# Optimization experiments

Hardware: AMD Instinct MI355X
Metric: run time of the kernel (lower is better)

The kernel has to match this reference:

```python
import jax, jax.numpy as jnp
from jax import lax
import numpy as np

EMA_ALPHA = 0.3
LN_EPS = 1e-5
SW = 5  # center_window_size


def _gelu(x):
    return jax.nn.gelu(x, approximate=False)  # torch nn.GELU default = exact erf


def _layernorm(x, g, b):
    mu = x.mean(-1, keepdims=True)
    var = ((x - mu) ** 2).mean(-1, keepdims=True)
    return (x - mu) * lax.rsqrt(var + LN_EPS) * g + b


def _ema_scan(x, alpha):
    # x: [B, T, C]; x_smooth[t] = lerp(x_smooth[t-1], x[t], alpha)
    x0 = x[:, 0]
    def step(prev, xt):
        s = prev + alpha * (xt - prev)
        return s, s
    _, ys = lax.scan(step, x0, jnp.swapaxes(x[:, 1:], 0, 1))  # [T-1, B, C]
    return jnp.concatenate([x0[:, None], jnp.swapaxes(ys, 0, 1)], axis=1)


def _lstm_dir(x, w_ih, w_hh, b):
    # x: [B, T, Cin]; w_ih: [Cin, 4H]; w_hh: [H, 4H]; b: [4H]. torch gate order i,f,g,o
    B = x.shape[0]
    H = w_hh.shape[0]
    pre = jnp.einsum('btc,ch->bth', x, w_ih) + b  # [B, T, 4H]
    def step(carry, p):
        h, c = carry
        gates = p + h @ w_hh
        i, f, g, o = jnp.split(gates, 4, axis=-1)
        c = jax.nn.sigmoid(f) * c + jax.nn.sigmoid(i) * jnp.tanh(g)
        h = jax.nn.sigmoid(o) * jnp.tanh(c)
        return (h, c), h
    init = (jnp.zeros((B, H), x.dtype), jnp.zeros((B, H), x.dtype))
    _, hs = lax.scan(step, init, jnp.swapaxes(pre, 0, 1))  # [T, B, H]
    return jnp.swapaxes(hs, 0, 1)


def _bilstm(x, wih_f, whh_f, b_f, wih_r, whh_r, b_r):
    fwd = _lstm_dir(x, wih_f, whh_f, b_f)
    bwd = jnp.flip(_lstm_dir(jnp.flip(x, axis=1), wih_r, whh_r, b_r), axis=1)
    return jnp.concatenate([fwd, bwd], axis=-1)  # [B, T, 2H]


def setup_inputs() -> dict:
    key = jax.random.key(0)
    ks = jax.random.split(key, 24)
    B, T, C, BD, O, H = 4096, 31, 768, 128, 12, 64
    AUG = 3 * BD  # 384
    def n(k, shape, s):
        return jax.random.normal(k, shape, dtype=jnp.float32) * s
    return {
        'x': n(ks[0], (B, T, C), 1.0),
        'cls_w': n(ks[1], (C, BD), 0.03), 'cls_b': jnp.zeros((BD,), jnp.float32),
        'delta_w': n(ks[2], (C, BD), 0.03), 'delta_b': jnp.zeros((BD,), jnp.float32),
        'acc_w': n(ks[3], (C, BD), 0.03), 'acc_b': jnp.zeros((BD,), jnp.float32),
        'cls_ln_g': jnp.ones((BD,), jnp.float32), 'cls_ln_b': jnp.zeros((BD,), jnp.float32),
        'delta_ln_g': jnp.ones((BD,), jnp.float32), 'delta_ln_b': jnp.zeros((BD,), jnp.float32),
        'acc_ln_g': jnp.ones((BD,), jnp.float32), 'acc_ln_b': jnp.zeros((BD,), jnp.float32),
        'lin0_w': n(ks[4], (AUG, 256), 0.05), 'lin0_b': jnp.zeros((256,), jnp.float32),
        'gate': jnp.float32(0.2),
        'attn_w': n(ks[5], (2 * H, 1), 0.08), 'attn_b': jnp.zeros((1,), jnp.float32),
        'attn_temp': jnp.float32(1.0),
        'lin1_w': n(ks[6], (C, O), 0.03), 'lin1_b': jnp.zeros((O,), jnp.float32),
        'lin2_w': n(ks[7], (2 * H, O), 0.08), 'lin2_b': jnp.zeros((O,), jnp.float32),
        'lstm_wih_f': n(ks[8], (256, 4 * H), 0.06), 'lstm_whh_f': n(ks[9], (H, 4 * H), 0.12),
        'lstm_b_f': jnp.zeros((4 * H,), jnp.float32),
        'lstm_wih_r': n(ks[10], (256, 4 * H), 0.06), 'lstm_whh_r': n(ks[11], (H, 4 * H), 0.12),
        'lstm_b_r': jnp.zeros((4 * H,), jnp.float32),
    }


def reference(x, cls_w, cls_b, delta_w, delta_b, acc_w, acc_b,
              cls_ln_g, cls_ln_b, delta_ln_g, delta_ln_b, acc_ln_g, acc_ln_b,
              lin0_w, lin0_b, gate, attn_w, attn_b, attn_temp,
              lin1_w, lin1_b, lin2_w, lin2_b,
              lstm_wih_f, lstm_whh_f, lstm_b_f, lstm_wih_r, lstm_whh_r, lstm_b_r):
    T = x.shape[1]
    hsl = T // 2
    l, r = max(0, hsl - SW), min(T, hsl + SW + 1)  # center window [10, 21) for T=31

    # --- robust deltas: EMA smoothing + reflect-padded finite differences ---
    x_smooth = _ema_scan(x, EMA_ALPHA)                       # [B, T, C]
    padded = jnp.pad(x_smooth, ((0, 0), (2, 0), (0, 0)), mode='reflect')  # [B, T+2, C]
    dx = padded[:, 1:] - padded[:, :-1]                       # [B, T+1, C]
    ddx = dx[:, 1:] - dx[:, :-1]                              # [B, T, C]
    delta_stream = dx[:, 1:]                                  # [B, T, C]
    acc_stream = ddx                                          # [B, T, C]

    # --- linear branch: mean of lin1 over center window of smoothed stream ---
    linear_logits = (x_smooth[:, l:r] @ lin1_w + lin1_b).mean(axis=1)  # [B, O]

    # --- bottlenecks (eval mode: dropout identity) + LayerNorms ---
    cls_bn = _layernorm(_gelu(x_smooth @ cls_w + cls_b), cls_ln_g, cls_ln_b)
    delta_bn = _layernorm(_gelu(delta_stream @ delta_w + delta_b), delta_ln_g, delta_ln_b)
    acc_bn = _layernorm(_gelu(acc_stream @ acc_w + acc_b), acc_ln_g, acc_ln_b)
    x_aug = jnp.concatenate([cls_bn, delta_bn, acc_bn], axis=-1)  # [B, T, 384]

    x_lstm = _gelu(x_aug @ lin0_w + lin0_b)                   # [B, T, 256]
    x_lstm = x_lstm - x_lstm.mean(axis=1, keepdims=True)      # center over time (fp32)

    # --- BiLSTM + attention pooling over center window ---
    lstm_out = _bilstm(x_lstm, lstm_wih_f, lstm_whh_f, lstm_b_f,
                       lstm_wih_r, lstm_whh_r, lstm_b_r)      # [B, T, 128]
    window = lstm_out[:, l:r]                                 # [B, W, 128]
    temp = jax.nn.softplus(attn_temp) + 0.001
    scores = (window @ attn_w + attn_b)[..., 0] / temp        # [B, W]
    attn = jax.nn.softmax(scores, axis=1)[..., None]          # [B, W, 1]
    attended = (attn * window).sum(axis=1)                    # [B, 128]
    lstm_logits = attended @ lin2_w + lin2_b                  # [B, O]

    g = jax.nn.sigmoid(gate)
    final_logits = linear_logits + g * (lstm_logits - linear_logits)
    return final_logits, attended
```

## Files before the change

kernel.cpp:

```cpp
#include <hip/hip_runtime.h>
#include <cstdint>
#include <cstddef>


typedef short s8v __attribute__((ext_vector_type(8)));
typedef float f4v __attribute__((ext_vector_type(4)));

__device__ __forceinline__ unsigned short f2bf(float f) {
  union { float f; unsigned int u; } v; v.f = f;
  unsigned int u = v.u;
  return (unsigned short)((u + 0x7fffu + ((u >> 16) & 1u)) >> 16);
}
__device__ __forceinline__ float bf2f(unsigned short h) {
  union { unsigned int u; float f; } v; v.u = ((unsigned int)h) << 16;
  return v.f;
}
__device__ __forceinline__ float fsig(float x) {
  return __fdividef(1.f, 1.f + __expf(-x));
}
__device__ __forceinline__ float ftanh(float x) {
  return 1.f - __fdividef(2.f, 1.f + __expf(2.f * x));
}
__device__ __forceinline__ float fgelu(float x) {
  return 0.5f * x * (1.f + erff(x * 0.70710678118654752f));
}

#define OFF_W1T   0u
#define OFF_W2T   589824u
#define OFF_WIHT  786432u
#define OFF_WHHT  1048576u
#define OFF_XS    1114112u
#define OFF_XW    196149248u
#define OFF_LL    208732160u
#define OFF_WIN   208928768u
#define OFF_XAUG  220463104u
#define OFF_XLSTM 317980672u

__global__ __launch_bounds__(256) void k0_prep(
    const float* __restrict__ cls_w, const float* __restrict__ delta_w,
    const float* __restrict__ acc_w, const float* __restrict__ lin0_w,
    const float* __restrict__ wih_f, const float* __restrict__ wih_r,
    const float* __restrict__ whh_f, const float* __restrict__ whh_r,
    unsigned short* __restrict__ ws) {
  int i = blockIdx.x * 256 + threadIdx.x;
  if (i < 294912) {
    int n = i / 768, k = i - n * 768;
    int seg = n >> 7, nn = n & 127;
    const float* w = seg == 0 ? cls_w : (seg == 1 ? delta_w : acc_w);
    ws[i] = f2bf(w[k * 128 + nn]);
  } else if (i < 393216) {
    int j = i - 294912;
    int n = j / 384, k = j - n * 384;
    ws[i] = f2bf(lin0_w[k * 256 + n]);
  } else if (i < 524288) {
    int j = i - 393216;
    int n = j >> 8, k = j & 255;
    ws[i] = f2bf(n < 256 ? wih_f[k * 256 + n] : wih_r[k * 256 + (n - 256)]);
  } else if (i < 557056) {
    int j = i - 524288;
    int d = j >> 14, rem = j & 16383;
    int n = rem >> 6, k = rem & 63;
    const float* w = d ? whh_r : whh_f;
    ws[i] = f2bf(w[k * 256 + n]);
  }
}

__global__ __launch_bounds__(256) void k1_ema(
    const float* __restrict__ x, unsigned short* __restrict__ xs,
    float* __restrict__ xw) {
  int gid = blockIdx.x * 256 + threadIdx.x;
  int b = gid / 768;
  int c = gid - b * 768;
  size_t base = (size_t)b * 31 * 768 + c;
  float s = x[base];
  xs[base] = f2bf(s);
  float wsum = 0.f;
#pragma unroll
  for (int t = 1; t < 31; ++t) {
    float xv = x[base + t * 768];
    s = s + 0.3f * (xv - s);
    xs[base + t * 768] = f2bf(s);
    if (t >= 10 && t <= 20) wsum += s;
  }
  xw[gid] = wsum * (1.f / 11.f);
}

__global__ __launch_bounds__(64) void k1b_linlog(
    const float* __restrict__ xw, const float* __restrict__ lin1_w,
    const float* __restrict__ lin1_b, float* __restrict__ ll) {
  int b = blockIdx.x;
  int lane = threadIdx.x;
  float p[12];
#pragma unroll
  for (int o = 0; o < 12; ++o) p[o] = 0.f;
  for (int k = lane; k < 768; k += 64) {
    float xv = xw[b * 768 + k];
    const float* w = lin1_w + k * 12;
#pragma unroll
    for (int o = 0; o < 12; ++o) p[o] += xv * w[o];
  }
#pragma unroll
  for (int o = 0; o < 12; ++o) {
    float v = p[o];
#pragma unroll
    for (int s = 1; s < 64; s <<= 1) v += __shfl_xor(v, s, 64);
    p[o] = v;
  }
  if (lane == 0) {
#pragma unroll
    for (int o = 0; o < 12; ++o) ll[b * 12 + o] = p[o] + lin1_b[o];
  }
}

template <int KDIM>
__device__ __forceinline__ void gemm64x128(
    const unsigned short* __restrict__ A, int rowClamp,
    const unsigned short* __restrict__ Bt,
    unsigned short* sA, unsigned short* sB, f4v acc[4][2]) {
  const int tid  = threadIdx.x;
  const int lane = tid & 63;
  const int wv   = tid >> 6;
  const int l15  = lane & 15;
  const int quad = lane >> 4;
#pragma unroll
  for (int mt = 0; mt < 4; ++mt)
#pragma unroll
    for (int nt = 0; nt < 2; ++nt)
      acc[mt][nt] = (f4v){0.f, 0.f, 0.f, 0.f};

  for (int kt = 0; kt < KDIM / 64; ++kt) {
#pragma unroll
    for (int c2 = 0; c2 < 2; ++c2) {
      int id = tid + c2 * 256;
      int row = id >> 3, kc = (id & 7) * 8;
      int gr = row < rowClamp ? row : rowClamp;
      uint4 v = *(const uint4*)(A + (size_t)gr * KDIM + kt * 64 + kc);
      *(uint4*)(&sA[row * 72 + kc]) = v;
    }
#pragma unroll
    for (int c2 = 0; c2 < 4; ++c2) {
      int id = tid + c2 * 256;
      int row = id >> 3, kc = (id & 7) * 8;
      uint4 v = *(const uint4*)(Bt + (size_t)row * KDIM + kt * 64 + kc);
      *(uint4*)(&sB[row * 72 + kc]) = v;
    }
    __syncthreads();
#pragma unroll
    for (int ks = 0; ks < 2; ++ks) {
      s8v af[4], bf[2];
#pragma unroll
      for (int mt = 0; mt < 4; ++mt)
        af[mt] = *(const s8v*)(&sA[(mt * 16 + l15) * 72 + ks * 32 + quad * 8]);
#pragma unroll
      for (int nt = 0; nt < 2; ++nt)
        bf[nt] = *(const s8v*)(&sB[(wv * 32 + nt * 16 + l15) * 72 + ks * 32 + quad * 8]);
#pragma unroll
      for (int mt = 0; mt < 4; ++mt)
#pragma unroll
        for (int nt = 0; nt < 2; ++nt)
          acc[mt][nt] = __builtin_amdgcn_mfma_f32_16x16x32_bf16(af[mt], bf[nt], acc[mt][nt], 0, 0, 0);
    }
    __syncthreads();
  }
}

__device__ __forceinline__ void dump_acc(f4v acc[4][2], float* sP) {
  const int tid  = threadIdx.x;
  const int lane = tid & 63;
  const int wv   = tid >> 6;
  const int l15  = lane & 15;
  const int quad = lane >> 4;
#pragma unroll
  for (int mt = 0; mt < 4; ++mt)
#pragma unroll
    for (int nt = 0; nt < 2; ++nt)
#pragma unroll
      for (int r = 0; r < 4; ++r)
        sP[(mt * 16 + quad * 4 + r) * 132 + wv * 32 + nt * 16 + l15] = acc[mt][nt][r];
}

__device__ __forceinline__ float stencil_gelu(const float* sP, int seg, int row, int t,
                                              int col, const float* __restrict__ bias) {
  const float* p = sP + row * 132 + col;
  float v;
  if (seg == 0) {
    v = p[0];
  } else if (seg == 1) {
    v = (t == 0) ? (p[0] - p[132]) : (p[0] - p[-132]);
  } else {
    if (t == 0)      v = p[0] - 2.f * p[132] + p[264];
    else if (t == 1) v = 2.f * (p[0] - p[-132]);
    else             v = p[0] - 2.f * p[-132] + p[-264];
  }
  return fgelu(v + bias[col]);
}

__global__ __launch_bounds__(256) void k2_aug(
    const unsigned short* __restrict__ xs, const unsigned short* __restrict__ W1t,
    const float* __restrict__ cls_b, const float* __restrict__ delta_b,
    const float* __restrict__ acc_b,
    const float* __restrict__ g0, const float* __restrict__ be0,
    const float* __restrict__ g1, const float* __restrict__ be1,
    const float* __restrict__ g2, const float* __restrict__ be2,
    unsigned short* __restrict__ xaug) {
  __shared__ unsigned short sA[64 * 72];
  __shared__ unsigned short sB[128 * 72];
  __shared__ float sP[64 * 132];
  __shared__ float sMu[64], sRs[64];
  int seg = blockIdx.y;
  int rowBase = blockIdx.x * 62;
  f4v acc[4][2];
  gemm64x128<768>(xs + (size_t)rowBase * 768, 61, W1t + (size_t)seg * 128 * 768, sA, sB, acc);
  dump_acc(acc, sP);
  __syncthreads();
  const float* bias = seg == 0 ? cls_b : (seg == 1 ? delta_b : acc_b);
  const float* lng  = seg == 0 ? g0 : (seg == 1 ? g1 : g2);
  const float* lnb  = seg == 0 ? be0 : (seg == 1 ? be1 : be2);
  int tid = threadIdx.x;
  {
    int row = tid >> 2, q = tid & 3;
    if (row < 62) {
      int bb = row >= 31 ? 1 : 0;
      int t  = row - bb * 31;
      float sum = 0.f, ss = 0.f;
      for (int i = 0; i < 32; ++i) {
        float v = stencil_gelu(sP, seg, row, t, q * 32 + i, bias);
        sum += v; ss += v * v;
      }
      sum += __shfl_xor(sum, 1, 64); sum += __shfl_xor(sum, 2, 64);
      ss  += __shfl_xor(ss,  1, 64); ss  += __shfl_xor(ss,  2, 64);
      float mu = sum * (1.f / 128.f);
      if (q == 0) { sMu[row] = mu; sRs[row] = rsqrtf(ss * (1.f / 128.f) - mu * mu + 1e-5f); }
    }
  }
  __syncthreads();
  for (int idx = tid; idx < 62 * 128; idx += 256) {
    int row = idx >> 7, col = idx & 127;
    int bb = row >= 31 ? 1 : 0;
    int t  = row - bb * 31;
    float v = stencil_gelu(sP, seg, row, t, col, bias);
    float o = (v - sMu[row]) * sRs[row] * lng[col] + lnb[col];
    xaug[(size_t)(rowBase + row) * 384 + seg * 128 + col] = f2bf(o);
  }
}

__global__ __launch_bounds__(256) void k3_lstm_in(
    const unsigned short* __restrict__ xaug, const unsigned short* __restrict__ W2t,
    const float* __restrict__ lin0_b, unsigned short* __restrict__ xlstm) {
  __shared__ unsigned short sA[64 * 72];
  __shared__ unsigned short sB[128 * 72];
  __shared__ float sP[64 * 132];
  __shared__ float sCM[256];
  int by = blockIdx.y;
  int rowBase = blockIdx.x * 62;
  f4v acc[4][2];
  gemm64x128<384>(xaug + (size_t)rowBase * 384, 61, W2t + (size_t)by * 128 * 384, sA, sB, acc);
  dump_acc(acc, sP);
  __syncthreads();
  int tid = threadIdx.x;
  for (int idx = tid; idx < 62 * 128; idx += 256) {
    int row = idx >> 7, col = idx & 127;
    sP[row * 132 + col] = fgelu(sP[row * 132 + col] + lin0_b[by * 128 + col]);
  }
  __syncthreads();
  {
    int bb = tid >> 7, col = tid & 127;
    float s = 0.f;
    for (int tr = 0; tr < 31; ++tr) s += sP[(bb * 31 + tr) * 132 + col];
    sCM[tid] = s * (1.f / 31.f);
  }
  __syncthreads();
  for (int idx = tid; idx < 62 * 128; idx += 256) {
    int row = idx >> 7, col = idx & 127;
    int bb = row >= 31 ? 1 : 0;
    float v = sP[row * 132 + col] - sCM[bb * 128 + col];
    xlstm[(size_t)(rowBase + row) * 256 + by * 128 + col] = f2bf(v);
  }
}

__global__ __launch_bounds__(256) void k3b_pre(
    const unsigned short* __restrict__ xlstm, const unsigned short* __restrict__ Wiht,
    const float* __restrict__ b_f, const float* __restrict__ b_r,
    unsigned short* __restrict__ pre) {
  __shared__ unsigned short sA[64 * 72];
  __shared__ unsigned short sB[128 * 72];
  __shared__ float sP[64 * 132];
  int by = blockIdx.y;
  int rowBase = blockIdx.x * 64;
  f4v acc[4][2];
  gemm64x128<256>(xlstm + (size_t)rowBase * 256, 63, Wiht + (size_t)by * 128 * 256, sA, sB, acc);
  dump_acc(acc, sP);
  __syncthreads();
  int tid = threadIdx.x;
  for (int idx = tid; idx < 64 * 128; idx += 256) {
    int row = idx >> 7, col = idx & 127;
    int gcol = by * 128 + col;
    float bias = gcol < 256 ? b_f[gcol] : b_r[gcol - 256];
    pre[(size_t)(rowBase + row) * 512 + gcol] = f2bf(sP[row * 132 + col] + bias);
  }
}

__global__ __launch_bounds__(256) void k4_lstm(
    const unsigned short* __restrict__ pre, const unsigned short* __restrict__ Whht,
    unsigned short* __restrict__ win) {
  __shared__ unsigned short sW[256 * 72];
  __shared__ unsigned short sH[16 * 72];
  __shared__ float sG[16 * 260];
  int tid = threadIdx.x;
  int dir = blockIdx.y;
  int b0  = blockIdx.x * 16;
  {
    const unsigned short* src = Whht + dir * 16384;
#pragma unroll
    for (int c = 0; c < 8; ++c) {
      int id = tid + c * 256;
      int row = id >> 3, kc = (id & 7) * 8;
      uint4 v = *(const uint4*)(src + row * 64 + kc);
      *(uint4*)(&sW[row * 72 + kc]) = v;
    }
  }
  for (int i = tid; i < 16 * 72; i += 256) sH[i] = 0;
  __syncthreads();

  const int lane = tid & 63, wv = tid >> 6, l15 = lane & 15, quad = lane >> 4;
  const int eb = tid >> 4, jb = (tid & 15) * 4;
  float cs[4] = {0.f, 0.f, 0.f, 0.f};

  for (int t = 0; t < 31; ++t) {
    f4v acc[4];
#pragma unroll
    for (int nt = 0; nt < 4; ++nt) acc[nt] = (f4v){0.f, 0.f, 0.f, 0.f};
#pragma unroll
    for (int ks = 0; ks < 2; ++ks) {
      s8v af = *(const s8v*)(&sH[l15 * 72 + ks * 32 + quad * 8]);
#pragma unroll
      for (int nt = 0; nt < 4; ++nt) {
        int n = wv * 64 + nt * 16 + l15;
        s8v bf = *(const s8v*)(&sW[n * 72 + ks * 32 + quad * 8]);
        acc[nt] = __builtin_amdgcn_mfma_f32_16x16x32_bf16(af, bf, acc[nt], 0, 0, 0);
      }
    }
#pragma unroll
    for (int nt = 0; nt < 4; ++nt)
#pragma unroll
      for (int r = 0; r < 4; ++r)
        sG[(quad * 4 + r) * 260 + wv * 64 + nt * 16 + l15] = acc[nt][r];
    __syncthreads();

    int tt = dir ? 30 - t : t;
    const unsigned short* prow = pre + ((size_t)(b0 + eb) * 31 + tt) * 512 + dir * 256;
    ushort4 pi = *(const ushort4*)(prow + jb);
    ushort4 pf = *(const ushort4*)(prow + 64 + jb);
    ushort4 pg = *(const ushort4*)(prow + 128 + jb);
    ushort4 po = *(const ushort4*)(prow + 192 + jb);
    const float* g = &sG[eb * 260];
    float hv[4];
#pragma unroll
    for (int jj = 0; jj < 4; ++jj) {
      int j = jb + jj;
      float vi = g[j]       + bf2f(jj == 0 ? pi.x : jj == 1 ? pi.y : jj == 2 ? pi.z : pi.w);
      float vf = g[64 + j]  + bf2f(jj == 0 ? pf.x : jj == 1 ? pf.y : jj == 2 ? pf.z : pf.w);
      float vg = g[128 + j] + bf2f(jj == 0 ? pg.x : jj == 1 ? pg.y : jj == 2 ? pg.z : pg.w);
      float vo = g[192 + j] + bf2f(jj == 0 ? po.x : jj == 1 ? po.y : jj == 2 ? po.z : po.w);
      float cc = fsig(vf) * cs[jj] + fsig(vi) * ftanh(vg);
      cs[jj] = cc;
      hv[jj] = fsig(vo) * ftanh(cc);
    }
    ushort4 hb;
    hb.x = f2bf(hv[0]); hb.y = f2bf(hv[1]); hb.z = f2bf(hv[2]); hb.w = f2bf(hv[3]);
    *(ushort4*)(&sH[eb * 72 + jb]) = hb;
    if (tt >= 10 && tt <= 20)
      *(ushort4*)(win + ((size_t)(b0 + eb) * 11 + (tt - 10)) * 128 + dir * 64 + jb) = hb;
    __syncthreads();
  }
}

__global__ __launch_bounds__(256) void k5_attn(
    const unsigned short* __restrict__ win, const float* __restrict__ attn_w,
    const float* __restrict__ attn_b, const float* __restrict__ attn_t,
    const float* __restrict__ lin2_w, const float* __restrict__ lin2_b,
    const float* __restrict__ linlog, const float* __restrict__ gate,
    float* __restrict__ out) {
  __shared__ unsigned short sWin[176 * 128];
  __shared__ float sAw[128];
  __shared__ float sSc[176];
  __shared__ float sAtt[16 * 128];
  int tid = threadIdx.x;
  int b0  = blockIdx.x * 16;
#pragma unroll
  for (int c = 0; c < 11; ++c) {
    int id = tid + c * 256;
    int row = id >> 4, kc = (id & 15) * 8;
    uint4 v = *(const uint4*)(win + ((size_t)b0 * 11 + row) * 128 + kc);
    *(uint4*)(&sWin[row * 128 + kc]) = v;
  }
  if (tid < 128) sAw[tid] = attn_w[tid];
  __syncthreads();
  if (tid < 176) {
    int b = tid / 11, wt = tid - b * 11;
    const unsigned short* w = &sWin[(b * 11 + wt) * 128];
    float dot = 0.f;
    for (int ch = 0; ch < 128; ++ch) dot += bf2f(w[ch]) * sAw[ch];
    float temp = logf(1.f + __expf(attn_t[0])) + 0.001f;
    sSc[tid] = (dot + attn_b[0]) / temp;
  }
  __syncthreads();
  if (tid < 16) {
    float m = -1e30f;
    for (int wt = 0; wt < 11; ++wt) m = fmaxf(m, sSc[tid * 11 + wt]);
    float e[11], sum = 0.f;
    for (int wt = 0; wt < 11; ++wt) { e[wt] = __expf(sSc[tid * 11 + wt] - m); sum += e[wt]; }
    float inv = __fdividef(1.f, sum);
    for (int wt = 0; wt < 11; ++wt) sSc[tid * 11 + wt] = e[wt] * inv;
  }
  __syncthreads();
#pragma unroll
  for (int p = 0; p < 8; ++p) {
    int task = tid + p * 256;
    int b = task >> 7, ch = task & 127;
    float a = 0.f;
    for (int wt = 0; wt < 11; ++wt)
      a += sSc[b * 11 + wt] * bf2f(sWin[(b * 11 + wt) * 128 + ch]);
    sAtt[b * 128 + ch] = a;
    out[49152 + (size_t)(b0 + b) * 128 + ch] = a;
  }
  __syncthreads();
  if (tid < 192) {
    int b = tid / 12, o = tid - b * 12;
    float dot = 0.f;
    for (int ch = 0; ch < 128; ++ch) dot += sAtt[b * 128 + ch] * lin2_w[ch * 12 + o];
    dot += lin2_b[o];
    float lin = linlog[(size_t)(b0 + b) * 12 + o];
    float gg = fsig(gate[0]);
    out[(size_t)(b0 + b) * 12 + o] = lin + gg * (dot - lin);
  }
}

extern "C" void kernel_launch(void* const* d_in, const int* in_sizes, int n_in,
                              void* d_out, int out_size, void* d_ws, size_t ws_size,
                              hipStream_t stream) {
  const float* x       = (const float*)d_in[0];
  const float* cls_w   = (const float*)d_in[1];
  const float* cls_b   = (const float*)d_in[2];
  const float* delta_w = (const float*)d_in[3];
  const float* delta_b = (const float*)d_in[4];
  const float* acc_w   = (const float*)d_in[5];
  const float* acc_b   = (const float*)d_in[6];
  const float* cls_g   = (const float*)d_in[7];
  const float* cls_be  = (const float*)d_in[8];
  const float* del_g   = (const float*)d_in[9];
  const float* del_be  = (const float*)d_in[10];
  const float* accg    = (const float*)d_in[11];
  const float* accbe   = (const float*)d_in[12];
  const float* lin0_b  = (const float*)d_in[14];
  const float* gate    = (const float*)d_in[15];
  const float* attn_w  = (const float*)d_in[16];
  const float* attn_b  = (const float*)d_in[17];
  const float* attn_t  = (const float*)d_in[18];
  const float* lin1_w  = (const float*)d_in[19];
  const float* lin1_b  = (const float*)d_in[20];
  const float* lin2_w  = (const float*)d_in[21];
  const float* lin2_b  = (const float*)d_in[22];
  const float* wih_f   = (const float*)d_in[23];
  const float* whh_f   = (const float*)d_in[24];
  const float* b_f     = (const float*)d_in[25];
  const float* wih_r   = (const float*)d_in[26];
  const float* whh_r   = (const float*)d_in[27];
  const float* b_r     = (const float*)d_in[28];
  const float* lin0_w  = (const float*)d_in[13];

  char* ws = (char*)d_ws;
  unsigned short* W1t   = (unsigned short*)(ws + OFF_W1T);
  unsigned short* W2t   = (unsigned short*)(ws + OFF_W2T);
  unsigned short* Wiht  = (unsigned short*)(ws + OFF_WIHT);
  unsigned short* Whht  = (unsigned short*)(ws + OFF_WHHT);
  unsigned short* XS    = (unsigned short*)(ws + OFF_XS);
  unsigned short* PRE   = XS;
  float*          XW    = (float*)(ws + OFF_XW);
  float*          LL    = (float*)(ws + OFF_LL);
  unsigned short* WIN   = (unsigned short*)(ws + OFF_WIN);
  unsigned short* XAUG  = (unsigned short*)(ws + OFF_XAUG);
  unsigned short* XLSTM = (unsigned short*)(ws + OFF_XLSTM);
  float* out = (float*)d_out;

  k0_prep<<<2176, 256, 0, stream>>>(cls_w, delta_w, acc_w, lin0_w, wih_f, wih_r,
                                    whh_f, whh_r, (unsigned short*)ws);
  k1_ema<<<12288, 256, 0, stream>>>(x, XS, XW);
  k1b_linlog<<<4096, 64, 0, stream>>>(XW, lin1_w, lin1_b, LL);
  k2_aug<<<dim3(2048, 3), 256, 0, stream>>>(XS, W1t, cls_b, delta_b, acc_b,
                                            cls_g, cls_be, del_g, del_be, accg, accbe, XAUG);
  k3_lstm_in<<<dim3(2048, 2), 256, 0, stream>>>(XAUG, W2t, lin0_b, XLSTM);
  k3b_pre<<<dim3(1984, 4), 256, 0, stream>>>(XLSTM, Wiht, b_f, b_r, PRE);
  k4_lstm<<<dim3(256, 2), 256, 0, stream>>>(PRE, Whht, WIN);
  k5_attn<<<256, 256, 0, stream>>>(WIN, attn_w, attn_b, attn_t, lin2_w, lin2_b,
                                   LL, gate, out);
}
```

Before: 1.259 ms.

## Enlarge GEMM tiles to 128x128 with register prefetch and prefetch LSTM pre-activations

The shared GEMM helper now computes 128x128 tiles, with each wave owning a 64x64 quadrant. The next K slice is prefetched into registers while MFMAs run on the current one, and the epilogue buffer aliases the A/B staging memory. k2, k3 and k3b now cover twice as many rows per block and process the epilogue in two chunks, with launch bounds asking for two blocks per CU. The LSTM step kernel loads the next timestep's pre-activations before the barrier, to hide global latency on the sequential path. The larger tiles cut redundant B-tile loads and raise MFMA work per load, at the cost of higher register pressure and half as many blocks.

Measured after the change: 1.745 ms. +38.6%, slower.

```diff
diff --git a/kernel.cpp b/kernel.cpp
--- a/kernel.cpp
+++ b/kernel.cpp
@@ -113,70 +113,103 @@
 }
 
 template <int KDIM>
-__device__ __forceinline__ void gemm64x128(
+__device__ __forceinline__ void gemm128(
     const unsigned short* __restrict__ A, int rowClamp,
     const unsigned short* __restrict__ Bt,
-    unsigned short* sA, unsigned short* sB, f4v acc[4][2]) {
+    unsigned short* sA, unsigned short* sB, f4v acc[4][4]) {
   const int tid  = threadIdx.x;
   const int lane = tid & 63;
   const int wv   = tid >> 6;
   const int l15  = lane & 15;
   const int quad = lane >> 4;
+  const int mh   = (wv >> 1) * 64;
+  const int nh   = (wv & 1) * 64;
+  const int kc   = (tid & 7) * 8;
+  const int r0   = tid >> 3;
+
+  const unsigned short* ap[4];
+  const unsigned short* bp[4];
+  unsigned short* la[4];
+  unsigned short* lb[4];
+#pragma unroll
+  for (int c = 0; c < 4; ++c) {
+    int row = r0 + c * 32;
+    int gr = row < rowClamp ? row : rowClamp;
+    ap[c] = A + (size_t)gr * KDIM + kc;
+    bp[c] = Bt + (size_t)row * KDIM + kc;
+    la[c] = sA + row * 72 + kc;
+    lb[c] = sB + row * 72 + kc;
+  }
 #pragma unroll
   for (int mt = 0; mt < 4; ++mt)
 #pragma unroll
-    for (int nt = 0; nt < 2; ++nt)
+    for (int nt = 0; nt < 4; ++nt)
       acc[mt][nt] = (f4v){0.f, 0.f, 0.f, 0.f};
 
-  for (int kt = 0; kt < KDIM / 64; ++kt) {
-#pragma unroll
-    for (int c2 = 0; c2 < 2; ++c2) {
-      int id = tid + c2 * 256;
-      int row = id >> 3, kc = (id & 7) * 8;
-      int gr = row < rowClamp ? row : rowClamp;
-      uint4 v = *(const uint4*)(A + (size_t)gr * KDIM + kt * 64 + kc);
-      *(uint4*)(&sA[row * 72 + kc]) = v;
-    }
-#pragma unroll
-    for (int c2 = 0; c2 < 4; ++c2) {
-      int id = tid + c2 * 256;
-      int row = id >> 3, kc = (id & 7) * 8;
-      uint4 v = *(const uint4*)(Bt + (size_t)row * KDIM + kt * 64 + kc);
-      *(uint4*)(&sB[row * 72 + kc]) = v;
-    }
-    __syncthreads();
+  uint4 ar[4], br[4];
+#pragma unroll
+  for (int c = 0; c < 4; ++c) ar[c] = *(const uint4*)(ap[c]);
+#pragma unroll
+  for (int c = 0; c < 4; ++c) br[c] = *(const uint4*)(bp[c]);
+#pragma unroll
+  for (int c = 0; c < 4; ++c) *(uint4*)(la[c]) = ar[c];
+#pragma unroll
+  for (int c = 0; c < 4; ++c) *(uint4*)(lb[c]) = br[c];
+  __syncthreads();
+
+  constexpr int KT = KDIM / 64;
+  for (int kt = 0; kt < KT; ++kt) {
+    if (kt + 1 < KT) {
+      int ko = (kt + 1) * 64;
+#pragma unroll
+      for (int c = 0; c < 4; ++c) ar[c] = *(const uint4*)(ap[c] + ko);
+#pragma unroll
+      for (int c = 0; c < 4; ++c) br[c] = *(const uint4*)(bp[c] + ko);
+    }
 #pragma unroll
     for (int ks = 0; ks < 2; ++ks) {
-      s8v af[4], bf[2];
+      s8v af[4], bfv[4];
 #pragma unroll
       for (int mt = 0; mt < 4; ++mt)
-        af[mt] = *(const s8v*)(&sA[(mt * 16 + l15) * 72 + ks * 32 + quad * 8]);
-#pragma unroll
-      for (int nt = 0; nt < 2; ++nt)
-        bf[nt] = *(const s8v*)(&sB[(wv * 32 + nt * 16 + l15) * 72 + ks * 32 + quad * 8]);
+        af[mt] = *(const s8v*)(&sA[(mh + mt * 16 + l15) * 72 + ks * 32 + quad * 8]);
+#pragma unroll
+      for (int nt = 0; nt < 4; ++nt)
+        bfv[nt] = *(const s8v*)(&sB[(nh + nt * 16 + l15) * 72 + ks * 32 + quad * 8]);
 #pragma unroll
       for (int mt = 0; mt < 4; ++mt)
 #pragma unroll
-        for (int nt = 0; nt < 2; ++nt)
-          acc[mt][nt] = __builtin_amdgcn_mfma_f32_16x16x32_bf16(af[mt], bf[nt], acc[mt][nt], 0, 0, 0);
-    }
-    __syncthreads();
-  }
-}
-
-__device__ __forceinline__ void dump_acc(f4v acc[4][2], float* sP) {
+        for (int nt = 0; nt < 4; ++nt)
+          acc[mt][nt] = __builtin_amdgcn_mfma_f32_16x16x32_bf16(af[mt], bfv[nt], acc[mt][nt], 0, 0, 0);
+    }
+    __syncthreads();
+    if (kt + 1 < KT) {
+#pragma unroll
+      for (int c = 0; c < 4; ++c) *(uint4*)(la[c]) = ar[c];
+#pragma unroll
+      for (int c = 0; c < 4; ++c) *(uint4*)(lb[c]) = br[c];
+      __syncthreads();
+    }
+  }
+}
+
+__device__ __forceinline__ void dump_chunk(f4v acc[4][4], float* sP, int lo, int nrows) {
   const int tid  = threadIdx.x;
   const int lane = tid & 63;
   const int wv   = tid >> 6;
   const int l15  = lane & 15;
   const int quad = lane >> 4;
+  const int mh   = (wv >> 1) * 64;
+  const int nh   = (wv & 1) * 64;
 #pragma unroll
   for (int mt = 0; mt < 4; ++mt)
 #pragma unroll
-    for (int nt = 0; nt < 2; ++nt)
-#pragma unroll
-      for (int r = 0; r < 4; ++r)
-        sP[(mt * 16 + quad * 4 + r) * 132 + wv * 32 + nt * 16 + l15] = acc[mt][nt][r];
+    for (int nt = 0; nt < 4; ++nt)
+#pragma unroll
+      for (int r = 0; r < 4; ++r) {
+        int rr = mh + mt * 16 + quad * 4 + r - lo;
+        if ((unsigned)rr < (unsigned)nrows)
+          sP[rr * 132 + nh + nt * 16 + l15] = acc[mt][nt][r];
+      }
 }
 
 __device__ __forceinline__ float stencil_gelu(const float* sP, int seg, int row, int t,
@@ -195,7 +228,7 @@
   return fgelu(v + bias[col]);
 }
 
-__global__ __launch_bounds__(256) void k2_aug(
+__global__ __launch_bounds__(256, 2) void k2_aug(
     const unsigned short* __restrict__ xs, const unsigned short* __restrict__ W1t,
     const float* __restrict__ cls_b, const float* __restrict__ delta_b,
     const float* __restrict__ acc_b,
@@ -203,28 +236,31 @@
     const float* __restrict__ g1, const float* __restrict__ be1,
     const float* __restrict__ g2, const float* __restrict__ be2,
     unsigned short* __restrict__ xaug) {
-  __shared__ unsigned short sA[64 * 72];
-  __shared__ unsigned short sB[128 * 72];
-  __shared__ float sP[64 * 132];
-  __shared__ float sMu[64], sRs[64];
+  __shared__ __align__(16) char smem[36864 + 640];
+  unsigned short* sA = (unsigned short*)smem;
+  unsigned short* sB = (unsigned short*)(smem + 18432);
+  float* sP  = (float*)smem;
+  float* sMu = (float*)(smem + 36864);
+  float* sRs = sMu + 62;
   int seg = blockIdx.y;
-  int rowBase = blockIdx.x * 62;
-  f4v acc[4][2];
-  gemm64x128<768>(xs + (size_t)rowBase * 768, 61, W1t + (size_t)seg * 128 * 768, sA, sB, acc);
-  dump_acc(acc, sP);
-  __syncthreads();
+  int rowBase = blockIdx.x * 124;
+  f4v acc[4][4];
+  gemm128<768>(xs + (size_t)rowBase * 768, 123, W1t + (size_t)seg * 128 * 768, sA, sB, acc);
   const float* bias = seg == 0 ? cls_b : (seg == 1 ? delta_b : acc_b);
   const float* lng  = seg == 0 ? g0 : (seg == 1 ? g1 : g2);
   const float* lnb  = seg == 0 ? be0 : (seg == 1 ? be1 : be2);
   int tid = threadIdx.x;
-  {
-    int row = tid >> 2, q = tid & 3;
-    if (row < 62) {
-      int bb = row >= 31 ? 1 : 0;
-      int t  = row - bb * 31;
+#pragma unroll
+  for (int ck = 0; ck < 2; ++ck) {
+    int lo = ck * 62;
+    dump_chunk(acc, sP, lo, 62);
+    __syncthreads();
+    if (tid < 248) {
+      int row = tid >> 2, q = tid & 3;
+      int t = row % 31;
       float sum = 0.f, ss = 0.f;
       for (int i = 0; i < 32; ++i) {
-        float v = stencil_gelu(sP, seg, row, t, q * 32 + i, bias);
+        float v = stencil_gelu(sP, seg, row, t, q + 4 * i, bias);
         sum += v; ss += v * v;
       }
       sum += __shfl_xor(sum, 1, 64); sum += __shfl_xor(sum, 2, 64);
@@ -232,71 +268,83 @@
       float mu = sum * (1.f / 128.f);
       if (q == 0) { sMu[row] = mu; sRs[row] = rsqrtf(ss * (1.f / 128.f) - mu * mu + 1e-5f); }
     }
-  }
-  __syncthreads();
-  for (int idx = tid; idx < 62 * 128; idx += 256) {
-    int row = idx >> 7, col = idx & 127;
-    int bb = row >= 31 ? 1 : 0;
-    int t  = row - bb * 31;
-    float v = stencil_gelu(sP, seg, row, t, col, bias);
-    float o = (v - sMu[row]) * sRs[row] * lng[col] + lnb[col];
-    xaug[(size_t)(rowBase + row) * 384 + seg * 128 + col] = f2bf(o);
-  }
-}
-
-__global__ __launch_bounds__(256) void k3_lstm_in(
+    __syncthreads();
+    for (int idx = tid; idx < 62 * 128; idx += 256) {
+      int row = idx >> 7, col = idx & 127;
+      int t = row % 31;
+      float v = stencil_gelu(sP, seg, row, t, col, bias);
+      float o = (v - sMu[row]) * sRs[row] * lng[col] + lnb[col];
+      xaug[(size_t)(rowBase + lo + row) * 384 + seg * 128 + col] = f2bf(o);
+    }
+    __syncthreads();
+  }
+}
+
+__global__ __launch_bounds__(256, 2) void k3_lstm_in(
     const unsigned short* __restrict__ xaug, const unsigned short* __restrict__ W2t,
     const float* __restrict__ lin0_b, unsigned short* __restrict__ xlstm) {
-  __shared__ unsigned short sA[64 * 72];
-  __shared__ unsigned short sB[128 * 72];
-  __shared__ float sP[64 * 132];
-  __shared__ float sCM[256];
+  __shared__ __align__(16) char smem[36864 + 1024];
+  unsigned short* sA = (unsigned short*)smem;
+  unsigned short* sB = (unsigned short*)(smem + 18432);
+  float* sP  = (float*)smem;
+  float* sCM = (float*)(smem + 36864);
   int by = blockIdx.y;
-  int rowBase = blockIdx.x * 62;
-  f4v acc[4][2];
-  gemm64x128<384>(xaug + (size_t)rowBase * 384, 61, W2t + (size_t)by * 128 * 384, sA, sB, acc);
-  dump_acc(acc, sP);
-  __syncthreads();
+  int rowBase = blockIdx.x * 124;
+  f4v acc[4][4];
+  gemm128<384>(xaug + (size_t)rowBase * 384, 123, W2t + (size_t)by * 128 * 384, sA, sB, acc);
   int tid = threadIdx.x;
-  for (int idx = tid; idx < 62 * 128; idx += 256) {
-    int row = idx >> 7, col = idx & 127;
-    sP[row * 132 + col] = fgelu(sP[row * 132 + col] + lin0_b[by * 128 + col]);
-  }
-  __syncthreads();
-  {
-    int bb = tid >> 7, col = tid & 127;
-    float s = 0.f;
-    for (int tr = 0; tr < 31; ++tr) s += sP[(bb * 31 + tr) * 132 + col];
-    sCM[tid] = s * (1.f / 31.f);
-  }
-  __syncthreads();
-  for (int idx = tid; idx < 62 * 128; idx += 256) {
-    int row = idx >> 7, col = idx & 127;
-    int bb = row >= 31 ? 1 : 0;
-    float v = sP[row * 132 + col] - sCM[bb * 128 + col];
-    xlstm[(size_t)(rowBase + row) * 256 + by * 128 + col] = f2bf(v);
-  }
-}
-
-__global__ __launch_bounds__(256) void k3b_pre(
+#pragma unroll
+  for (int ck = 0; ck < 2; ++ck) {
+    int lo = ck * 62;
+    dump_chunk(acc, sP, lo, 62);
+    __syncthreads();
+    for (int idx = tid; idx < 62 * 128; idx += 256) {
+      int row = idx >> 7, col = idx & 127;
+      sP[row * 132 + col] = fgelu(sP[row * 132 + col] + lin0_b[by * 128 + col]);
+    }
+    __syncthreads();
+    {
+      int bb = tid >> 7, col = tid & 127;
+      float s = 0.f;
+      for (int tr = 0; tr < 31; ++tr) s += sP[(bb * 31 + tr) * 132 + col];
+      sCM[tid] = s * (1.f / 31.f);
+    }
+    __syncthreads();
+    for (int idx = tid; idx < 62 * 128; idx += 256) {
+      int row = idx >> 7, col = idx & 127;
+      int bb = row >= 31 ? 1 : 0;
+      float v = sP[row * 132 + col] - sCM[bb * 128 + col];
+      xlstm[(size_t)(rowBase + lo + row) * 256 + by * 128 + col] = f2bf(v);
+    }
+    __syncthreads();
+  }
+}
+
+__global__ __launch_bounds__(256, 2) void k3b_pre(
     const unsigned short* __restrict__ xlstm, const unsigned short* __restrict__ Wiht,
     const float* __restrict__ b_f, const float* __restrict__ b_r,
     unsigned short* __restrict__ pre) {
-  __shared__ unsigned short sA[64 * 72];
-  __shared__ unsigned short sB[128 * 72];
-  __shared__ float sP[64 * 132];
+  __shared__ __align__(16) char smem[36864];
+  unsigned short* sA = (unsigned short*)smem;
+  unsigned short* sB = (unsigned short*)(smem + 18432);
+  float* sP = (float*)smem;
   int by = blockIdx.y;
-  int rowBase = blockIdx.x * 64;
-  f4v acc[4][2];
-  gemm64x128<256>(xlstm + (size_t)rowBase * 256, 63, Wiht + (size_t)by * 128 * 256, sA, sB, acc);
-  dump_acc(acc, sP);
-  __syncthreads();
+  int rowBase = blockIdx.x * 128;
+  f4v acc[4][4];
+  gemm128<256>(xlstm + (size_t)rowBase * 256, 127, Wiht + (size_t)by * 128 * 256, sA, sB, acc);
   int tid = threadIdx.x;
-  for (int idx = tid; idx < 64 * 128; idx += 256) {
-    int row = idx >> 7, col = idx & 127;
-    int gcol = by * 128 + col;
-    float bias = gcol < 256 ? b_f[gcol] : b_r[gcol - 256];
-    pre[(size_t)(rowBase + row) * 512 + gcol] = f2bf(sP[row * 132 + col] + bias);
+#pragma unroll
+  for (int ck = 0; ck < 2; ++ck) {
+    int lo = ck * 64;
+    dump_chunk(acc, sP, lo, 64);
+    __syncthreads();
+    for (int idx = tid; idx < 64 * 128; idx += 256) {
+      int row = idx >> 7, col = idx & 127;
+      int gcol = by * 128 + col;
+      float bias = gcol < 256 ? b_f[gcol] : b_r[gcol - 256];
+      pre[(size_t)(rowBase + lo + row) * 512 + gcol] = f2bf(sP[row * 132 + col] + bias);
+    }
+    __syncthreads();
   }
 }
 
@@ -326,6 +374,13 @@
   const int eb = tid >> 4, jb = (tid & 15) * 4;
   float cs[4] = {0.f, 0.f, 0.f, 0.f};
 
+  int tt0 = dir ? 30 : 0;
+  const unsigned short* pbase = pre + ((size_t)(b0 + eb) * 31) * 512 + dir * 256;
+  ushort4 pi = *(const ushort4*)(pbase + tt0 * 512 + jb);
+  ushort4 pf = *(const ushort4*)(pbase + tt0 * 512 + 64 + jb);
+  ushort4 pg = *(const ushort4*)(pbase + tt0 * 512 + 128 + jb);
+  ushort4 po = *(const ushort4*)(pbase + tt0 * 512 + 192 + jb);
+
   for (int t = 0; t < 31; ++t) {
     f4v acc[4];
 #pragma unroll
@@ -336,8 +391,8 @@
 #pragma unroll
       for (int nt = 0; nt < 4; ++nt) {
         int n = wv * 64 + nt * 16 + l15;
-        s8v bf = *(const s8v*)(&sW[n * 72 + ks * 32 + quad * 8]);
-        acc[nt] = __builtin_amdgcn_mfma_f32_16x16x32_bf16(af, bf, acc[nt], 0, 0, 0);
+        s8v bfv = *(const s8v*)(&sW[n * 72 + ks * 32 + quad * 8]);
+        acc[nt] = __builtin_amdgcn_mfma_f32_16x16x32_bf16(af, bfv, acc[nt], 0, 0, 0);
       }
     }
 #pragma unroll
@@ -345,14 +400,18 @@
 #pragma unroll
       for (int r = 0; r < 4; ++r)
         sG[(quad * 4 + r) * 260 + wv * 64 + nt * 16 + l15] = acc[nt][r];
+
+    ushort4 ni, nf, ng, no;
+    if (t < 30) {
+      int ttn = dir ? 29 - t : t + 1;
+      ni = *(const ushort4*)(pbase + ttn * 512 + jb);
+      nf = *(const ushort4*)(pbase + ttn * 512 + 64 + jb);
+      ng = *(const ushort4*)(pbase + ttn * 512 + 128 + jb);
+      no = *(const ushort4*)(pbase + ttn * 512 + 192 + jb);
+    }
     __syncthreads();
 
     int tt = dir ? 30 - t : t;
-    const unsigned short* prow = pre + ((size_t)(b0 + eb) * 31 + tt) * 512 + dir * 256;
-    ushort4 pi = *(const ushort4*)(prow + jb);
-    ushort4 pf = *(const ushort4*)(prow + 64 + jb);
-    ushort4 pg = *(const ushort4*)(prow + 128 + jb);
-    ushort4 po = *(const ushort4*)(prow + 192 + jb);
     const float* g = &sG[eb * 260];
     float hv[4];
 #pragma unroll
@@ -371,6 +430,7 @@
     *(ushort4*)(&sH[eb * 72 + jb]) = hb;
     if (tt >= 10 && tt <= 20)
       *(ushort4*)(win + ((size_t)(b0 + eb) * 11 + (tt - 10)) * 128 + dir * 64 + jb) = hb;
+    if (t < 30) { pi = ni; pf = nf; pg = ng; po = no; }
     __syncthreads();
   }
 }
@@ -452,6 +512,7 @@
   const float* del_be  = (const float*)d_in[10];
   const float* accg    = (const float*)d_in[11];
   const float* accbe   = (const float*)d_in[12];
+  const float* lin0_w  = (const float*)d_in[13];
   const float* lin0_b  = (const float*)d_in[14];
   const float* gate    = (const float*)d_in[15];
   const float* attn_w  = (const float*)d_in[16];
@@ -467,7 +528,6 @@
   const float* wih_r   = (const float*)d_in[26];
   const float* whh_r   = (const float*)d_in[27];
   const float* b_r     = (const float*)d_in[28];
-  const float* lin0_w  = (const float*)d_in[13];
 
   char* ws = (char*)d_ws;
   unsigned short* W1t   = (unsigned short*)(ws + OFF_W1T);
@@ -487,10 +547,10 @@
                                     whh_f, whh_r, (unsigned short*)ws);
   k1_ema<<<12288, 256, 0, stream>>>(x, XS, XW);
   k1b_linlog<<<4096, 64, 0, stream>>>(XW, lin1_w, lin1_b, LL);
-  k2_aug<<<dim3(2048, 3), 256, 0, stream>>>(XS, W1t, cls_b, delta_b, acc_b,
+  k2_aug<<<dim3(1024, 3), 256, 0, stream>>>(XS, W1t, cls_b, delta_b, acc_b,
                                             cls_g, cls_be, del_g, del_be, accg, accbe, XAUG);
-  k3_lstm_in<<<dim3(2048, 2), 256, 0, stream>>>(XAUG, W2t, lin0_b, XLSTM);
-  k3b_pre<<<dim3(1984, 4), 256, 0, stream>>>(XLSTM, Wiht, b_f, b_r, PRE);
+  k3_lstm_in<<<dim3(1024, 2), 256, 0, stream>>>(XAUG, W2t, lin0_b, XLSTM);
+  k3b_pre<<<dim3(992, 4), 256, 0, stream>>>(XLSTM, Wiht, b_f, b_r, PRE);
   k4_lstm<<<dim3(256, 2), 256, 0, stream>>>(PRE, Whht, WIN);
   k5_attn<<<256, 256, 0, stream>>>(WIN, attn_w, attn_b, attn_t, lin2_w, lin2_b,
                                    LL, gate, out);
```
